# Kernel tuning notes

Measured on AMD Instinct MI355X. Metric: run time of the kernel, lower is better.

The kernel has to match this reference:

```python
import jax, jax.numpy as jnp
import numpy as np

HEAD_SIZE = 128
BLOCK_SIZE = 2048


def setup_inputs() -> dict:
    key = jax.random.key(0)
    k1, k2 = jax.random.split(key)
    B, T, D = 8, 2048, 1024
    x = jax.random.normal(k1, (B, T, D), dtype=jnp.float32)
    # Linear(dim, 3*head_size, bias=False): weight [3*head_size, dim], applied as x @ W.T
    W_qkv = jax.random.normal(k2, (3 * HEAD_SIZE, D), dtype=jnp.float32) * (1.0 / np.sqrt(D))
    return {"x": x, "W_qkv": W_qkv}


def reference(x, W_qkv):
    B, T, D = x.shape
    qkv = jnp.einsum('btd,hd->bth', x, W_qkv)  # [B, T, 3*head_size]
    q = qkv[:, :, :HEAD_SIZE]
    k = qkv[:, :, HEAD_SIZE:2 * HEAD_SIZE]
    v = qkv[:, :, 2 * HEAD_SIZE:]
    scale = 1.0 / np.sqrt(HEAD_SIZE).astype(np.float32)
    score = jnp.einsum('bqh,bkh->bqk', q, k) * scale  # [B, T, T]
    causal = jnp.tril(jnp.ones((T, T), dtype=bool))
    score = jnp.where(causal, score, -jnp.inf)
    attn = jax.nn.softmax(score, axis=-1)
    # dropout p=0.0 (eval) -> identity
    return jnp.einsum('bqk,bkh->bqh', attn, v)  # [B, T, head_size]
```

## Files before the change

kernel.cpp:

```cpp
#include <hip/hip_runtime.h>
#include <hip/hip_bf16.h>
#include <math.h>

#define D_MODEL 1024
#define TLEN    2048

typedef __attribute__((ext_vector_type(8))) short short8;
typedef __attribute__((ext_vector_type(4))) float f32x4;

static __device__ __forceinline__ unsigned short f2bf(float f) {
    __hip_bfloat16 h = __float2bfloat16(f);
    return __builtin_bit_cast(unsigned short, h);
}
static __device__ __forceinline__ float bf2f(unsigned short u) {
    unsigned int x = ((unsigned int)u) << 16;
    return __builtin_bit_cast(float, x);
}
static __device__ __forceinline__ void lds_cp16(void* lds, const void* g) {
    __builtin_amdgcn_global_load_lds(
        (const __attribute__((address_space(1))) unsigned int*)g,
        (__attribute__((address_space(3))) unsigned int*)lds, 16, 0, 0);
}

__global__ __launch_bounds__(256) void pack_w(const float* __restrict__ W,
                                              unsigned short* __restrict__ wt) {
    const int id = blockIdx.x * 256 + threadIdx.x;
    const int h  = id >> 7;
    const int kg = id & 127;
    const int k0 = kg * 8;
    const int kt = k0 >> 6;
    const int kin = k0 & 63;
    const int np = h >> 7;
    const int hp = h & 127;
    const float4 a = *(const float4*)&W[(size_t)h * D_MODEL + k0];
    const float4 b = *(const float4*)&W[(size_t)h * D_MODEL + k0 + 4];
    short8 v;
    v[0] = (short)f2bf(a.x); v[1] = (short)f2bf(a.y);
    v[2] = (short)f2bf(a.z); v[3] = (short)f2bf(a.w);
    v[4] = (short)f2bf(b.x); v[5] = (short)f2bf(b.y);
    v[6] = (short)f2bf(b.z); v[7] = (short)f2bf(b.w);
    const size_t dst = ((size_t)(np * 16 + kt) * 128 + hp) * 64 + (kin ^ ((hp & 7) * 8));
    *(short8*)&wt[dst] = v;
}

__global__ __launch_bounds__(256, 4) void qkv_gemm(const float* __restrict__ x,
                                                   const unsigned short* __restrict__ wt,
                                                   unsigned short* __restrict__ qk,
                                                   unsigned short* __restrict__ vt) {
    __shared__ unsigned short As[64][88];
    __shared__ unsigned short Bs[128 * 64];

    const int tid  = threadIdx.x;
    const int lane = tid & 63;
    const int w    = tid >> 6;
    const int wm   = w >> 1, wn = w & 1;
    const int cc   = lane & 15, g = lane >> 4;
    const int row0 = blockIdx.x * 64;
    const int np   = blockIdx.y;

    const int xr  = tid >> 2;
    const int xc0 = (tid & 3) * 16;

    const f32x4 zero = {0.f, 0.f, 0.f, 0.f};
    f32x4 acc[2][4];
#pragma unroll
    for (int i = 0; i < 2; ++i)
#pragma unroll
        for (int j = 0; j < 4; ++j) acc[i][j] = zero;

    const float* xrow = x + (size_t)(row0 + xr) * D_MODEL + xc0;
    float4 xa[4];
#pragma unroll
    for (int i = 0; i < 4; ++i) xa[i] = *(const float4*)(xrow + i * 4);

    const unsigned short* wtile0 =
        wt + (size_t)np * 16 * 128 * 64 + (w * 4 * 1024 + lane * 16) / 2;
    unsigned short* bdst = Bs + (w * 4 * 1024) / 2;

    for (int kt = 0; kt < 16; ++kt) {
        __syncthreads();
        {
            short8 s0, s1;
            s0[0] = (short)f2bf(xa[0].x); s0[1] = (short)f2bf(xa[0].y);
            s0[2] = (short)f2bf(xa[0].z); s0[3] = (short)f2bf(xa[0].w);
            s0[4] = (short)f2bf(xa[1].x); s0[5] = (short)f2bf(xa[1].y);
            s0[6] = (short)f2bf(xa[1].z); s0[7] = (short)f2bf(xa[1].w);
            s1[0] = (short)f2bf(xa[2].x); s1[1] = (short)f2bf(xa[2].y);
            s1[2] = (short)f2bf(xa[2].z); s1[3] = (short)f2bf(xa[2].w);
            s1[4] = (short)f2bf(xa[3].x); s1[5] = (short)f2bf(xa[3].y);
            s1[6] = (short)f2bf(xa[3].z); s1[7] = (short)f2bf(xa[3].w);
            *(short8*)&As[xr][xc0]     = s0;
            *(short8*)&As[xr][xc0 + 8] = s1;
        }
        const unsigned short* wtk = wtile0 + (size_t)kt * 128 * 64;
#pragma unroll
        for (int i = 0; i < 4; ++i)
            lds_cp16(bdst + i * 512, wtk + i * 512);
        __syncthreads();

        short8 af[2][2], bf[2][4];
#pragma unroll
        for (int ks = 0; ks < 2; ++ks) {
#pragma unroll
            for (int mt = 0; mt < 2; ++mt)
                af[ks][mt] = *(const short8*)&As[wm * 32 + mt * 16 + cc][ks * 32 + g * 8];
#pragma unroll
            for (int nt = 0; nt < 4; ++nt) {
                const int h = wn * 64 + nt * 16 + cc;
                bf[ks][nt] = *(const short8*)&Bs[h * 64 + (((ks * 4 + g) ^ (h & 7)) << 3)];
            }
        }
        if (kt + 1 < 16) {
#pragma unroll
            for (int i = 0; i < 4; ++i)
                xa[i] = *(const float4*)(xrow + (kt + 1) * 64 + i * 4);
        }
        __builtin_amdgcn_s_setprio(1);
#pragma unroll
        for (int ks = 0; ks < 2; ++ks)
#pragma unroll
            for (int mt = 0; mt < 2; ++mt)
#pragma unroll
                for (int nt = 0; nt < 4; ++nt)
                    acc[mt][nt] = __builtin_amdgcn_mfma_f32_16x16x32_bf16(
                        af[ks][mt], bf[ks][nt], acc[mt][nt], 0, 0, 0);
        __builtin_amdgcn_s_setprio(0);
    }

    const int bb  = row0 >> 11;
    const int tr0 = row0 & 2047;
    const float qs = (np == 0) ? 0.08838834764831845f : 1.0f;
#pragma unroll
    for (int mt = 0; mt < 2; ++mt)
#pragma unroll
        for (int nt = 0; nt < 4; ++nt) {
            const int colp = wn * 64 + nt * 16;
            if (np < 2) {
#pragma unroll
                for (int r = 0; r < 4; ++r) {
                    const int row = row0 + wm * 32 + mt * 16 + g * 4 + r;
                    qk[(size_t)row * 256 + np * 128 + colp + cc] = f2bf(acc[mt][nt][r] * qs);
                }
            } else {
                const int d    = colp + cc;
                const int trow = tr0 + wm * 32 + mt * 16 + g * 4;
                ushort4 u;
                u.x = f2bf(acc[mt][nt][0]);
                u.y = f2bf(acc[mt][nt][1]);
                u.z = f2bf(acc[mt][nt][2]);
                u.w = f2bf(acc[mt][nt][3]);
                *(ushort4*)&vt[((size_t)(bb * 128 + d)) * TLEN + trow] = u;
            }
        }
}

__global__ __launch_bounds__(256, 3) void attn_part(const unsigned short* __restrict__ qk,
                                                    const unsigned short* __restrict__ vt,
                                                    unsigned short* __restrict__ po,
                                                    float2* __restrict__ ml) {
    __shared__ unsigned short Ks[64 * 128];
    __shared__ unsigned short Vs[128 * 64];
    __shared__ unsigned short Ps[4][16][72];

    const int tid  = threadIdx.x;
    const int lane = tid & 63;
    const int w    = tid >> 6;
    const int cc   = lane & 15, g = lane >> 4;
    const int bx   = blockIdx.x;
    const int qt   = 31 - (bx / 3);
    const int ggg  = bx % 3;
    const int b    = blockIdx.y;
    const int q0   = qt * 64;
    const int slot = (b * 32 + qt) * 3 + ggg;
    const int n    = qt + 1;
    const int cnt  = (n > ggg) ? ((n - ggg + 2) / 3) : 0;

    if (cnt == 0) {
#pragma unroll
        for (int nt = 0; nt < 8; ++nt)
#pragma unroll
            for (int r = 0; r < 4; ++r)
                po[((size_t)slot * 64 + w * 16 + g * 4 + r) * 128 + nt * 16 + cc] = 0;
        if (g == 0) ml[slot * 64 + w * 16 + cc] = make_float2(-INFINITY, 0.f);
        return;
    }

    short8 qf[4];
    {
        const unsigned short* qb =
            qk + ((size_t)(b * TLEN + q0 + w * 16 + cc)) * 256 + g * 8;
#pragma unroll
        for (int kt = 0; kt < 4; ++kt) qf[kt] = *(const short8*)(qb + kt * 32);
    }

    const f32x4 zero = {0.f, 0.f, 0.f, 0.f};
    f32x4 o[8];
#pragma unroll
    for (int nt = 0; nt < 8; ++nt) o[nt] = zero;
    float mrun = -INFINITY, lrun = 0.f;

    int koff[4], voff[2];
#pragma unroll
    for (int kt = 0; kt < 4; ++kt)
        koff[kt] = cc * 128 + (((kt * 4 + g) ^ (cc & 7)) << 3);
#pragma unroll
    for (int ks = 0; ks < 2; ++ks)
        voff[ks] = cc * 64 + (((ks * 4 + g) ^ (cc & 7)) << 3);

    const int kRow = tid >> 2;
    const int kG0  = (tid & 3) * 4;
    const int vRow = tid >> 1;
    const int vG0  = (tid & 1) * 4;
    const unsigned short* kgp = qk + ((size_t)(b * TLEN + kRow)) * 256 + 128 + kG0 * 8;
    const unsigned short* vgp = vt + ((size_t)(b * 128 + vRow)) * TLEN + vG0 * 8;

    short8 kr[4], vr[4];
#pragma unroll
    for (int i = 0; i < 4; ++i) kr[i] = *(const short8*)(kgp + (size_t)ggg * 16384 + i * 8);
#pragma unroll
    for (int i = 0; i < 4; ++i) vr[i] = *(const short8*)(vgp + ggg * 64 + i * 8);

    for (int s = 0; s < cnt; ++s) {
        const int t  = 3 * s + ggg;
        const int j0 = t * 64;
        __syncthreads();
#pragma unroll
        for (int i = 0; i < 4; ++i) {
            *(short8*)&Ks[kRow * 128 + (((kG0 + i) ^ (kRow & 7)) << 3)] = kr[i];
            *(short8*)&Vs[vRow * 64  + (((vG0 + i) ^ (vRow & 7)) << 3)] = vr[i];
        }
        __syncthreads();
        if (s + 1 < cnt) {
            const int tn = t + 3;
#pragma unroll
            for (int i = 0; i < 4; ++i) kr[i] = *(const short8*)(kgp + (size_t)tn * 16384 + i * 8);
#pragma unroll
            for (int i = 0; i < 4; ++i) vr[i] = *(const short8*)(vgp + tn * 64 + i * 8);
        }

        f32x4 st[4];
#pragma unroll
        for (int jt = 0; jt < 4; ++jt) st[jt] = zero;
        __builtin_amdgcn_s_setprio(1);
#pragma unroll
        for (int kt = 0; kt < 4; ++kt)
#pragma unroll
            for (int jt = 0; jt < 4; ++jt) {
                const short8 kf = *(const short8*)&Ks[koff[kt] + jt * 2048];
                st[jt] = __builtin_amdgcn_mfma_f32_16x16x32_bf16(kf, qf[kt], st[jt], 0, 0, 0);
            }
        __builtin_amdgcn_s_setprio(0);

        if (t == qt) {
            const int qg = q0 + w * 16 + cc;
            const int jb = j0 + 4 * g;
#pragma unroll
            for (int jt = 0; jt < 4; ++jt)
#pragma unroll
                for (int r = 0; r < 4; ++r)
                    if (jb + jt * 16 + r > qg) st[jt][r] = -INFINITY;
        }
        float pmax = -INFINITY;
#pragma unroll
        for (int jt = 0; jt < 4; ++jt) {
            const float a = fmaxf(st[jt][0], st[jt][1]);
            const float c = fmaxf(st[jt][2], st[jt][3]);
            pmax = fmaxf(pmax, fmaxf(a, c));
        }
        pmax = fmaxf(pmax, __shfl_xor(pmax, 16));
        pmax = fmaxf(pmax, __shfl_xor(pmax, 32));

        if (!__all(pmax <= mrun + 8.f)) {
            const float newm  = fmaxf(mrun, pmax);
            const float alpha = __expf(mrun - newm);
            mrun = newm;
            lrun *= alpha;
            float arow[4];
#pragma unroll
            for (int r = 0; r < 4; ++r) arow[r] = __shfl(alpha, 20 * g + r);
#pragma unroll
            for (int nt = 0; nt < 8; ++nt)
#pragma unroll
                for (int r = 0; r < 4; ++r) o[nt][r] *= arow[r];
        }

        float rs = 0.f;
#pragma unroll
        for (int jt = 0; jt < 4; ++jt) {
            const float p0 = __expf(st[jt][0] - mrun);
            const float p1 = __expf(st[jt][1] - mrun);
            const float p2 = __expf(st[jt][2] - mrun);
            const float p3 = __expf(st[jt][3] - mrun);
            rs += (p0 + p1) + (p2 + p3);
            uint2 pw;
            pw.x = (unsigned int)f2bf(p0) | ((unsigned int)f2bf(p1) << 16);
            pw.y = (unsigned int)f2bf(p2) | ((unsigned int)f2bf(p3) << 16);
            *(uint2*)&Ps[w][cc][jt * 16 + 4 * g] = pw;
        }
        rs += __shfl_xor(rs, 16);
        rs += __shfl_xor(rs, 32);
        lrun += rs;

        asm volatile("s_waitcnt lgkmcnt(0)" ::: "memory");
        __builtin_amdgcn_sched_barrier(0);

        __builtin_amdgcn_s_setprio(1);
#pragma unroll
        for (int ks = 0; ks < 2; ++ks) {
            const short8 pa = *(const short8*)&Ps[w][cc][ks * 32 + g * 8];
#pragma unroll
            for (int nt = 0; nt < 8; ++nt) {
                const short8 vf = *(const short8*)&Vs[voff[ks] + nt * 1024];
                o[nt] = __builtin_amdgcn_mfma_f32_16x16x32_bf16(pa, vf, o[nt], 0, 0, 0);
            }
        }
        __builtin_amdgcn_s_setprio(0);
    }

#pragma unroll
    for (int nt = 0; nt < 8; ++nt)
#pragma unroll
        for (int r = 0; r < 4; ++r)
            po[((size_t)slot * 64 + w * 16 + g * 4 + r) * 128 + nt * 16 + cc] =
                f2bf(o[nt][r]);
    if (g == 0) ml[slot * 64 + w * 16 + cc] = make_float2(mrun, lrun);
}

__global__ __launch_bounds__(256) void attn_merge(const unsigned short* __restrict__ po,
                                                  const float2* __restrict__ ml,
                                                  float* __restrict__ out) {
    const int bq   = blockIdx.x;
    const int row  = threadIdx.x >> 2;
    const int cs   = (threadIdx.x & 3) * 32;
    const int slot = bq * 3;

    const float2 ml0 = ml[(size_t)(slot + 0) * 64 + row];
    const float2 ml1 = ml[(size_t)(slot + 1) * 64 + row];
    const float2 ml2 = ml[(size_t)(slot + 2) * 64 + row];
    const float M  = fmaxf(fmaxf(ml0.x, ml1.x), ml2.x);
    float e0 = __expf(ml0.x - M);
    float e1 = __expf(ml1.x - M);
    float e2 = __expf(ml2.x - M);
    const float inv = 1.f / (ml0.y * e0 + ml1.y * e1 + ml2.y * e2);
    e0 *= inv; e1 *= inv; e2 *= inv;

    const unsigned short* p0 = po + ((size_t)(slot + 0) * 64 + row) * 128 + cs;
    const unsigned short* p1 = po + ((size_t)(slot + 1) * 64 + row) * 128 + cs;
    const unsigned short* p2 = po + ((size_t)(slot + 2) * 64 + row) * 128 + cs;
    float* op = out + ((size_t)bq * 64 + row) * 128 + cs;

#pragma unroll
    for (int i = 0; i < 4; ++i) {
        const short8 a = *(const short8*)(p0 + i * 8);
        const short8 b = *(const short8*)(p1 + i * 8);
        const short8 c = *(const short8*)(p2 + i * 8);
        float4 o0, o1;
        o0.x = bf2f((unsigned short)a[0]) * e0 + bf2f((unsigned short)b[0]) * e1 + bf2f((unsigned short)c[0]) * e2;
        o0.y = bf2f((unsigned short)a[1]) * e0 + bf2f((unsigned short)b[1]) * e1 + bf2f((unsigned short)c[1]) * e2;
        o0.z = bf2f((unsigned short)a[2]) * e0 + bf2f((unsigned short)b[2]) * e1 + bf2f((unsigned short)c[2]) * e2;
        o0.w = bf2f((unsigned short)a[3]) * e0 + bf2f((unsigned short)b[3]) * e1 + bf2f((unsigned short)c[3]) * e2;
        o1.x = bf2f((unsigned short)a[4]) * e0 + bf2f((unsigned short)b[4]) * e1 + bf2f((unsigned short)c[4]) * e2;
        o1.y = bf2f((unsigned short)a[5]) * e0 + bf2f((unsigned short)b[5]) * e1 + bf2f((unsigned short)c[5]) * e2;
        o1.z = bf2f((unsigned short)a[6]) * e0 + bf2f((unsigned short)b[6]) * e1 + bf2f((unsigned short)c[6]) * e2;
        o1.w = bf2f((unsigned short)a[7]) * e0 + bf2f((unsigned short)b[7]) * e1 + bf2f((unsigned short)c[7]) * e2;
        *(float4*)(op + i * 8)     = o0;
        *(float4*)(op + i * 8 + 4) = o1;
    }
}

extern "C" void kernel_launch(void* const* d_in, const int* in_sizes, int n_in,
                              void* d_out, int out_size, void* d_ws, size_t ws_size,
                              hipStream_t stream) {
    (void)in_sizes; (void)n_in; (void)out_size; (void)ws_size;
    const float* x = (const float*)d_in[0];
    const float* W = (const float*)d_in[1];
    float* out = (float*)d_out;

    unsigned short* qkbf = (unsigned short*)d_ws;
    unsigned short* vtbf = qkbf + (size_t)16384 * 256;
    unsigned short* wtbf = vtbf + (size_t)8 * 128 * 2048;
    unsigned short* pobf = wtbf + (size_t)3 * 16 * 128 * 64;
    float2*         mlf  = (float2*)(pobf + (size_t)768 * 64 * 128);

    pack_w<<<dim3(192), 256, 0, stream>>>(W, wtbf);
    qkv_gemm<<<dim3(256, 3), 256, 0, stream>>>(x, wtbf, qkbf, vtbf);
    attn_part<<<dim3(96, 8), 256, 0, stream>>>(qkbf, vtbf, pobf, mlf);
    attn_merge<<<dim3(256), 256, 0, stream>>>(pobf, mlf, out);
}
```

Before: 66.78 us.

## Fuse split-KV merge into attention kernel via last-block atomic counter

Removes the separate attn_merge launch. Each of the three split blocks for a query tile bumps an atomic counter when it finishes, and the last one to arrive does the softmax-weighted merge of the partial outputs and writes the fp32 result. This saves a kernel launch and the gap between kernels, at the cost of a memset launch, an extra block barrier and fence, and some tail work on the last-arriving blocks.

```diff
diff --git a/kernel.cpp b/kernel.cpp
--- a/kernel.cpp
+++ b/kernel.cpp
@@ -157,10 +157,13 @@
 __global__ __launch_bounds__(256, 3) void attn_part(const unsigned short* __restrict__ qk,
                                                     const unsigned short* __restrict__ vt,
                                                     unsigned short* __restrict__ po,
-                                                    float2* __restrict__ ml) {
+                                                    float2* __restrict__ ml,
+                                                    float* __restrict__ out,
+                                                    int* __restrict__ cnt_g) {
     __shared__ unsigned short Ks[64 * 128];
     __shared__ unsigned short Vs[128 * 64];
     __shared__ unsigned short Ps[4][16][72];
+    __shared__ int lastflag;
 
     const int tid  = threadIdx.x;
     const int lane = tid & 63;
@@ -171,7 +174,8 @@
     const int ggg  = bx % 3;
     const int b    = blockIdx.y;
     const int q0   = qt * 64;
-    const int slot = (b * 32 + qt) * 3 + ggg;
+    const int bq   = b * 32 + qt;
+    const int slot = bq * 3 + ggg;
     const int n    = qt + 1;
     const int cnt  = (n > ggg) ? ((n - ggg + 2) / 3) : 0;
 
@@ -182,161 +186,167 @@
             for (int r = 0; r < 4; ++r)
                 po[((size_t)slot * 64 + w * 16 + g * 4 + r) * 128 + nt * 16 + cc] = 0;
         if (g == 0) ml[slot * 64 + w * 16 + cc] = make_float2(-INFINITY, 0.f);
-        return;
+    } else {
+        short8 qf[4];
+        {
+            const unsigned short* qb =
+                qk + ((size_t)(b * TLEN + q0 + w * 16 + cc)) * 256 + g * 8;
+#pragma unroll
+            for (int kt = 0; kt < 4; ++kt) qf[kt] = *(const short8*)(qb + kt * 32);
+        }
+
+        const f32x4 zero = {0.f, 0.f, 0.f, 0.f};
+        f32x4 o[8];
+#pragma unroll
+        for (int nt = 0; nt < 8; ++nt) o[nt] = zero;
+        float mrun = -INFINITY, lrun = 0.f;
+
+        int koff[4], voff[2];
+#pragma unroll
+        for (int kt = 0; kt < 4; ++kt)
+            koff[kt] = cc * 128 + (((kt * 4 + g) ^ (cc & 7)) << 3);
+#pragma unroll
+        for (int ks = 0; ks < 2; ++ks)
+            voff[ks] = cc * 64 + (((ks * 4 + g) ^ (cc & 7)) << 3);
+
+        const int kRow = tid >> 2;
+        const int kG0  = (tid & 3) * 4;
+        const int vRow = tid >> 1;
+        const int vG0  = (tid & 1) * 4;
+        const unsigned short* kgp = qk + ((size_t)(b * TLEN + kRow)) * 256 + 128 + kG0 * 8;
+        const unsigned short* vgp = vt + ((size_t)(b * 128 + vRow)) * TLEN + vG0 * 8;
+
+        short8 kr[4], vr[4];
+#pragma unroll
+        for (int i = 0; i < 4; ++i) kr[i] = *(const short8*)(kgp + (size_t)ggg * 16384 + i * 8);
+#pragma unroll
+        for (int i = 0; i < 4; ++i) vr[i] = *(const short8*)(vgp + ggg * 64 + i * 8);
+
+        for (int s = 0; s < cnt; ++s) {
+            const int t  = 3 * s + ggg;
+            const int j0 = t * 64;
+            __syncthreads();
+#pragma unroll
+            for (int i = 0; i < 4; ++i) {
+                *(short8*)&Ks[kRow * 128 + (((kG0 + i) ^ (kRow & 7)) << 3)] = kr[i];
+                *(short8*)&Vs[vRow * 64  + (((vG0 + i) ^ (vRow & 7)) << 3)] = vr[i];
+            }
+            __syncthreads();
+            if (s + 1 < cnt) {
+                const int tn = t + 3;
+#pragma unroll
+                for (int i = 0; i < 4; ++i) kr[i] = *(const short8*)(kgp + (size_t)tn * 16384 + i * 8);
+#pragma unroll
+                for (int i = 0; i < 4; ++i) vr[i] = *(const short8*)(vgp + tn * 64 + i * 8);
+            }
+
+            f32x4 st[4];
+#pragma unroll
+            for (int jt = 0; jt < 4; ++jt) st[jt] = zero;
+            __builtin_amdgcn_s_setprio(1);
+#pragma unroll
+            for (int kt = 0; kt < 4; ++kt)
+#pragma unroll
+                for (int jt = 0; jt < 4; ++jt) {
+                    const short8 kf = *(const short8*)&Ks[koff[kt] + jt * 2048];
+                    st[jt] = __builtin_amdgcn_mfma_f32_16x16x32_bf16(kf, qf[kt], st[jt], 0, 0, 0);
+                }
+            __builtin_amdgcn_s_setprio(0);
+
+            if (t == qt) {
+                const int qg = q0 + w * 16 + cc;
+                const int jb = j0 + 4 * g;
+#pragma unroll
+                for (int jt = 0; jt < 4; ++jt)
+#pragma unroll
+                    for (int r = 0; r < 4; ++r)
+                        if (jb + jt * 16 + r > qg) st[jt][r] = -INFINITY;
+            }
+            float pmax = -INFINITY;
+#pragma unroll
+            for (int jt = 0; jt < 4; ++jt) {
+                const float a = fmaxf(st[jt][0], st[jt][1]);
+                const float c = fmaxf(st[jt][2], st[jt][3]);
+                pmax = fmaxf(pmax, fmaxf(a, c));
+            }
+            pmax = fmaxf(pmax, __shfl_xor(pmax, 16));
+            pmax = fmaxf(pmax, __shfl_xor(pmax, 32));
+
+            if (!__all(pmax <= mrun + 8.f)) {
+                const float newm  = fmaxf(mrun, pmax);
+                const float alpha = __expf(mrun - newm);
+                mrun = newm;
+                lrun *= alpha;
+                float arow[4];
+#pragma unroll
+                for (int r = 0; r < 4; ++r) arow[r] = __shfl(alpha, 20 * g + r);
+#pragma unroll
+                for (int nt = 0; nt < 8; ++nt)
+#pragma unroll
+                    for (int r = 0; r < 4; ++r) o[nt][r] *= arow[r];
+            }
+
+            float rs = 0.f;
+#pragma unroll
+            for (int jt = 0; jt < 4; ++jt) {
+                const float p0 = __expf(st[jt][0] - mrun);
+                const float p1 = __expf(st[jt][1] - mrun);
+                const float p2 = __expf(st[jt][2] - mrun);
+                const float p3 = __expf(st[jt][3] - mrun);
+                rs += (p0 + p1) + (p2 + p3);
+                uint2 pw;
+                pw.x = (unsigned int)f2bf(p0) | ((unsigned int)f2bf(p1) << 16);
+                pw.y = (unsigned int)f2bf(p2) | ((unsigned int)f2bf(p3) << 16);
+                *(uint2*)&Ps[w][cc][jt * 16 + 4 * g] = pw;
+            }
+            rs += __shfl_xor(rs, 16);
+            rs += __shfl_xor(rs, 32);
+            lrun += rs;
+
+            asm volatile("s_waitcnt lgkmcnt(0)" ::: "memory");
+            __builtin_amdgcn_sched_barrier(0);
+
+            __builtin_amdgcn_s_setprio(1);
+#pragma unroll
+            for (int ks = 0; ks < 2; ++ks) {
+                const short8 pa = *(const short8*)&Ps[w][cc][ks * 32 + g * 8];
+#pragma unroll
+                for (int nt = 0; nt < 8; ++nt) {
+                    const short8 vf = *(const short8*)&Vs[voff[ks] + nt * 1024];
+                    o[nt] = __builtin_amdgcn_mfma_f32_16x16x32_bf16(pa, vf, o[nt], 0, 0, 0);
+                }
+            }
+            __builtin_amdgcn_s_setprio(0);
+        }
+
+#pragma unroll
+        for (int nt = 0; nt < 8; ++nt)
+#pragma unroll
+            for (int r = 0; r < 4; ++r)
+                po[((size_t)slot * 64 + w * 16 + g * 4 + r) * 128 + nt * 16 + cc] =
+                    f2bf(o[nt][r]);
+        if (g == 0) ml[slot * 64 + w * 16 + cc] = make_float2(mrun, lrun);
     }
 
-    short8 qf[4];
-    {
-        const unsigned short* qb =
-            qk + ((size_t)(b * TLEN + q0 + w * 16 + cc)) * 256 + g * 8;
-#pragma unroll
-        for (int kt = 0; kt < 4; ++kt) qf[kt] = *(const short8*)(qb + kt * 32);
+    __syncthreads();
+    if (tid == 0) {
+        __threadfence();
+        const int old = __hip_atomic_fetch_add(&cnt_g[bq], 1,
+                                               __ATOMIC_ACQ_REL,
+                                               __HIP_MEMORY_SCOPE_AGENT);
+        lastflag = (old == 2) ? 1 : 0;
     }
-
-    const f32x4 zero = {0.f, 0.f, 0.f, 0.f};
-    f32x4 o[8];
-#pragma unroll
-    for (int nt = 0; nt < 8; ++nt) o[nt] = zero;
-    float mrun = -INFINITY, lrun = 0.f;
-
-    int koff[4], voff[2];
-#pragma unroll
-    for (int kt = 0; kt < 4; ++kt)
-        koff[kt] = cc * 128 + (((kt * 4 + g) ^ (cc & 7)) << 3);
-#pragma unroll
-    for (int ks = 0; ks < 2; ++ks)
-        voff[ks] = cc * 64 + (((ks * 4 + g) ^ (cc & 7)) << 3);
-
-    const int kRow = tid >> 2;
-    const int kG0  = (tid & 3) * 4;
-    const int vRow = tid >> 1;
-    const int vG0  = (tid & 1) * 4;
-    const unsigned short* kgp = qk + ((size_t)(b * TLEN + kRow)) * 256 + 128 + kG0 * 8;
-    const unsigned short* vgp = vt + ((size_t)(b * 128 + vRow)) * TLEN + vG0 * 8;
-
-    short8 kr[4], vr[4];
-#pragma unroll
-    for (int i = 0; i < 4; ++i) kr[i] = *(const short8*)(kgp + (size_t)ggg * 16384 + i * 8);
-#pragma unroll
-    for (int i = 0; i < 4; ++i) vr[i] = *(const short8*)(vgp + ggg * 64 + i * 8);
-
-    for (int s = 0; s < cnt; ++s) {
-        const int t  = 3 * s + ggg;
-        const int j0 = t * 64;
-        __syncthreads();
-#pragma unroll
-        for (int i = 0; i < 4; ++i) {
-            *(short8*)&Ks[kRow * 128 + (((kG0 + i) ^ (kRow & 7)) << 3)] = kr[i];
-            *(short8*)&Vs[vRow * 64  + (((vG0 + i) ^ (vRow & 7)) << 3)] = vr[i];
-        }
-        __syncthreads();
-        if (s + 1 < cnt) {
-            const int tn = t + 3;
-#pragma unroll
-            for (int i = 0; i < 4; ++i) kr[i] = *(const short8*)(kgp + (size_t)tn * 16384 + i * 8);
-#pragma unroll
-            for (int i = 0; i < 4; ++i) vr[i] = *(const short8*)(vgp + tn * 64 + i * 8);
-        }
-
-        f32x4 st[4];
-#pragma unroll
-        for (int jt = 0; jt < 4; ++jt) st[jt] = zero;
-        __builtin_amdgcn_s_setprio(1);
-#pragma unroll
-        for (int kt = 0; kt < 4; ++kt)
-#pragma unroll
-            for (int jt = 0; jt < 4; ++jt) {
-                const short8 kf = *(const short8*)&Ks[koff[kt] + jt * 2048];
-                st[jt] = __builtin_amdgcn_mfma_f32_16x16x32_bf16(kf, qf[kt], st[jt], 0, 0, 0);
-            }
-        __builtin_amdgcn_s_setprio(0);
-
-        if (t == qt) {
-            const int qg = q0 + w * 16 + cc;
-            const int jb = j0 + 4 * g;
-#pragma unroll
-            for (int jt = 0; jt < 4; ++jt)
-#pragma unroll
-                for (int r = 0; r < 4; ++r)
-                    if (jb + jt * 16 + r > qg) st[jt][r] = -INFINITY;
-        }
-        float pmax = -INFINITY;
-#pragma unroll
-        for (int jt = 0; jt < 4; ++jt) {
-            const float a = fmaxf(st[jt][0], st[jt][1]);
-            const float c = fmaxf(st[jt][2], st[jt][3]);
-            pmax = fmaxf(pmax, fmaxf(a, c));
-        }
-        pmax = fmaxf(pmax, __shfl_xor(pmax, 16));
-        pmax = fmaxf(pmax, __shfl_xor(pmax, 32));
-
-        if (!__all(pmax <= mrun + 8.f)) {
-            const float newm  = fmaxf(mrun, pmax);
-            const float alpha = __expf(mrun - newm);
-            mrun = newm;
-            lrun *= alpha;
-            float arow[4];
-#pragma unroll
-            for (int r = 0; r < 4; ++r) arow[r] = __shfl(alpha, 20 * g + r);
-#pragma unroll
-            for (int nt = 0; nt < 8; ++nt)
-#pragma unroll
-                for (int r = 0; r < 4; ++r) o[nt][r] *= arow[r];
-        }
-
-        float rs = 0.f;
-#pragma unroll
-        for (int jt = 0; jt < 4; ++jt) {
-            const float p0 = __expf(st[jt][0] - mrun);
-            const float p1 = __expf(st[jt][1] - mrun);
-            const float p2 = __expf(st[jt][2] - mrun);
-            const float p3 = __expf(st[jt][3] - mrun);
-            rs += (p0 + p1) + (p2 + p3);
-            uint2 pw;
-            pw.x = (unsigned int)f2bf(p0) | ((unsigned int)f2bf(p1) << 16);
-            pw.y = (unsigned int)f2bf(p2) | ((unsigned int)f2bf(p3) << 16);
-            *(uint2*)&Ps[w][cc][jt * 16 + 4 * g] = pw;
-        }
-        rs += __shfl_xor(rs, 16);
-        rs += __shfl_xor(rs, 32);
-        lrun += rs;
-
-        asm volatile("s_waitcnt lgkmcnt(0)" ::: "memory");
-        __builtin_amdgcn_sched_barrier(0);
-
-        __builtin_amdgcn_s_setprio(1);
-#pragma unroll
-        for (int ks = 0; ks < 2; ++ks) {
-            const short8 pa = *(const short8*)&Ps[w][cc][ks * 32 + g * 8];
-#pragma unroll
-            for (int nt = 0; nt < 8; ++nt) {
-                const short8 vf = *(const short8*)&Vs[voff[ks] + nt * 1024];
-                o[nt] = __builtin_amdgcn_mfma_f32_16x16x32_bf16(pa, vf, o[nt], 0, 0, 0);
-            }
-        }
-        __builtin_amdgcn_s_setprio(0);
-    }
-
-#pragma unroll
-    for (int nt = 0; nt < 8; ++nt)
-#pragma unroll
-        for (int r = 0; r < 4; ++r)
-            po[((size_t)slot * 64 + w * 16 + g * 4 + r) * 128 + nt * 16 + cc] =
-                f2bf(o[nt][r]);
-    if (g == 0) ml[slot * 64 + w * 16 + cc] = make_float2(mrun, lrun);
-}
-
-__global__ __launch_bounds__(256) void attn_merge(const unsigned short* __restrict__ po,
-                                                  const float2* __restrict__ ml,
-                                                  float* __restrict__ out) {
-    const int bq   = blockIdx.x;
-    const int row  = threadIdx.x >> 2;
-    const int cs   = (threadIdx.x & 3) * 32;
-    const int slot = bq * 3;
-
-    const float2 ml0 = ml[(size_t)(slot + 0) * 64 + row];
-    const float2 ml1 = ml[(size_t)(slot + 1) * 64 + row];
-    const float2 ml2 = ml[(size_t)(slot + 2) * 64 + row];
+    __syncthreads();
+    if (lastflag == 0) return;
+    __threadfence();
+
+    const int row  = tid >> 2;
+    const int cs   = (tid & 3) * 32;
+    const int sl0  = bq * 3;
+
+    const float2 ml0 = ml[(size_t)(sl0 + 0) * 64 + row];
+    const float2 ml1 = ml[(size_t)(sl0 + 1) * 64 + row];
+    const float2 ml2 = ml[(size_t)(sl0 + 2) * 64 + row];
     const float M  = fmaxf(fmaxf(ml0.x, ml1.x), ml2.x);
     float e0 = __expf(ml0.x - M);
     float e1 = __expf(ml1.x - M);
@@ -344,25 +354,25 @@
     const float inv = 1.f / (ml0.y * e0 + ml1.y * e1 + ml2.y * e2);
     e0 *= inv; e1 *= inv; e2 *= inv;
 
-    const unsigned short* p0 = po + ((size_t)(slot + 0) * 64 + row) * 128 + cs;
-    const unsigned short* p1 = po + ((size_t)(slot + 1) * 64 + row) * 128 + cs;
-    const unsigned short* p2 = po + ((size_t)(slot + 2) * 64 + row) * 128 + cs;
+    const unsigned short* p0 = po + ((size_t)(sl0 + 0) * 64 + row) * 128 + cs;
+    const unsigned short* p1 = po + ((size_t)(sl0 + 1) * 64 + row) * 128 + cs;
+    const unsigned short* p2 = po + ((size_t)(sl0 + 2) * 64 + row) * 128 + cs;
     float* op = out + ((size_t)bq * 64 + row) * 128 + cs;
 
 #pragma unroll
     for (int i = 0; i < 4; ++i) {
         const short8 a = *(const short8*)(p0 + i * 8);
-        const short8 b = *(const short8*)(p1 + i * 8);
+        const short8 bb = *(const short8*)(p1 + i * 8);
         const short8 c = *(const short8*)(p2 + i * 8);
         float4 o0, o1;
-        o0.x = bf2f((unsigned short)a[0]) * e0 + bf2f((unsigned short)b[0]) * e1 + bf2f((unsigned short)c[0]) * e2;
-        o0.y = bf2f((unsigned short)a[1]) * e0 + bf2f((unsigned short)b[1]) * e1 + bf2f((unsigned short)c[1]) * e2;
-        o0.z = bf2f((unsigned short)a[2]) * e0 + bf2f((unsigned short)b[2]) * e1 + bf2f((unsigned short)c[2]) * e2;
-        o0.w = bf2f((unsigned short)a[3]) * e0 + bf2f((unsigned short)b[3]) * e1 + bf2f((unsigned short)c[3]) * e2;
-        o1.x = bf2f((unsigned short)a[4]) * e0 + bf2f((unsigned short)b[4]) * e1 + bf2f((unsigned short)c[4]) * e2;
-        o1.y = bf2f((unsigned short)a[5]) * e0 + bf2f((unsigned short)b[5]) * e1 + bf2f((unsigned short)c[5]) * e2;
-        o1.z = bf2f((unsigned short)a[6]) * e0 + bf2f((unsigned short)b[6]) * e1 + bf2f((unsigned short)c[6]) * e2;
-        o1.w = bf2f((unsigned short)a[7]) * e0 + bf2f((unsigned short)b[7]) * e1 + bf2f((unsigned short)c[7]) * e2;
+        o0.x = bf2f((unsigned short)a[0]) * e0 + bf2f((unsigned short)bb[0]) * e1 + bf2f((unsigned short)c[0]) * e2;
+        o0.y = bf2f((unsigned short)a[1]) * e0 + bf2f((unsigned short)bb[1]) * e1 + bf2f((unsigned short)c[1]) * e2;
+        o0.z = bf2f((unsigned short)a[2]) * e0 + bf2f((unsigned short)bb[2]) * e1 + bf2f((unsigned short)c[2]) * e2;
+        o0.w = bf2f((unsigned short)a[3]) * e0 + bf2f((unsigned short)bb[3]) * e1 + bf2f((unsigned short)c[3]) * e2;
+        o1.x = bf2f((unsigned short)a[4]) * e0 + bf2f((unsigned short)bb[4]) * e1 + bf2f((unsigned short)c[4]) * e2;
+        o1.y = bf2f((unsigned short)a[5]) * e0 + bf2f((unsigned short)bb[5]) * e1 + bf2f((unsigned short)c[5]) * e2;
+        o1.z = bf2f((unsigned short)a[6]) * e0 + bf2f((unsigned short)bb[6]) * e1 + bf2f((unsigned short)c[6]) * e2;
+        o1.w = bf2f((unsigned short)a[7]) * e0 + bf2f((unsigned short)bb[7]) * e1 + bf2f((unsigned short)c[7]) * e2;
         *(float4*)(op + i * 8)     = o0;
         *(float4*)(op + i * 8 + 4) = o1;
     }
@@ -381,9 +391,10 @@
     unsigned short* wtbf = vtbf + (size_t)8 * 128 * 2048;
     unsigned short* pobf = wtbf + (size_t)3 * 16 * 128 * 64;
     float2*         mlf  = (float2*)(pobf + (size_t)768 * 64 * 128);
-
+    int*            cntg = (int*)(mlf + (size_t)768 * 64);
+
+    hipMemsetAsync(cntg, 0, 256 * sizeof(int), stream);
     pack_w<<<dim3(192), 256, 0, stream>>>(W, wtbf);
     qkv_gemm<<<dim3(256, 3), 256, 0, stream>>>(x, wtbf, qkbf, vtbf);
-    attn_part<<<dim3(96, 8), 256, 0, stream>>>(qkbf, vtbf, pobf, mlf);
-    attn_merge<<<dim3(256), 256, 0, stream>>>(pobf, mlf, out);
-}
+    attn_part<<<dim3(96, 8), 256, 0, stream>>>(qkbf, vtbf, pobf, mlf, out, cntg);
+}
```

After: 195.2 us. 192% more time.

## Load QKV GEMM B operand directly to registers, double-buffer A in LDS

Applied to the files above, without the earlier changes.

The weight operand of the QKV projection GEMM is now kept row-major in bf16 and each lane loads its MFMA B fragments straight from global memory into registers, prefetching the next k-tile. The swizzled LDS staging tile for B is removed. The A tile is double-buffered in LDS so one barrier per iteration suffices. This saves LDS traffic and a sync, at the cost of more registers (launch bounds lowered to 3 waves) and uncoalesced 16-byte global reads of W per lane.

```diff
diff --git a/kernel.cpp b/kernel.cpp
--- a/kernel.cpp
+++ b/kernel.cpp
@@ -16,22 +16,12 @@
     unsigned int x = ((unsigned int)u) << 16;
     return __builtin_bit_cast(float, x);
 }
-static __device__ __forceinline__ void lds_cp16(void* lds, const void* g) {
-    __builtin_amdgcn_global_load_lds(
-        (const __attribute__((address_space(1))) unsigned int*)g,
-        (__attribute__((address_space(3))) unsigned int*)lds, 16, 0, 0);
-}
 
 __global__ __launch_bounds__(256) void pack_w(const float* __restrict__ W,
-                                              unsigned short* __restrict__ wt) {
+                                              unsigned short* __restrict__ wb) {
     const int id = blockIdx.x * 256 + threadIdx.x;
     const int h  = id >> 7;
-    const int kg = id & 127;
-    const int k0 = kg * 8;
-    const int kt = k0 >> 6;
-    const int kin = k0 & 63;
-    const int np = h >> 7;
-    const int hp = h & 127;
+    const int k0 = (id & 127) * 8;
     const float4 a = *(const float4*)&W[(size_t)h * D_MODEL + k0];
     const float4 b = *(const float4*)&W[(size_t)h * D_MODEL + k0 + 4];
     short8 v;
@@ -39,16 +29,14 @@
     v[2] = (short)f2bf(a.z); v[3] = (short)f2bf(a.w);
     v[4] = (short)f2bf(b.x); v[5] = (short)f2bf(b.y);
     v[6] = (short)f2bf(b.z); v[7] = (short)f2bf(b.w);
-    const size_t dst = ((size_t)(np * 16 + kt) * 128 + hp) * 64 + (kin ^ ((hp & 7) * 8));
-    *(short8*)&wt[dst] = v;
-}
-
-__global__ __launch_bounds__(256, 4) void qkv_gemm(const float* __restrict__ x,
-                                                   const unsigned short* __restrict__ wt,
+    *(short8*)&wb[(size_t)h * D_MODEL + k0] = v;
+}
+
+__global__ __launch_bounds__(256, 3) void qkv_gemm(const float* __restrict__ x,
+                                                   const unsigned short* __restrict__ wb,
                                                    unsigned short* __restrict__ qk,
                                                    unsigned short* __restrict__ vt) {
-    __shared__ unsigned short As[64][88];
-    __shared__ unsigned short Bs[128 * 64];
+    __shared__ unsigned short As[2][64][88];
 
     const int tid  = threadIdx.x;
     const int lane = tid & 63;
@@ -73,12 +61,20 @@
 #pragma unroll
     for (int i = 0; i < 4; ++i) xa[i] = *(const float4*)(xrow + i * 4);
 
-    const unsigned short* wtile0 =
-        wt + (size_t)np * 16 * 128 * 64 + (w * 4 * 1024 + lane * 16) / 2;
-    unsigned short* bdst = Bs + (w * 4 * 1024) / 2;
+    const unsigned short* bptr[4];
+#pragma unroll
+    for (int nt = 0; nt < 4; ++nt)
+        bptr[nt] = wb + (size_t)(np * 128 + wn * 64 + nt * 16 + cc) * D_MODEL + g * 8;
+
+    short8 bq[2][2][4];
+#pragma unroll
+    for (int ks = 0; ks < 2; ++ks)
+#pragma unroll
+        for (int nt = 0; nt < 4; ++nt)
+            bq[0][ks][nt] = *(const short8*)(bptr[nt] + ks * 32);
 
     for (int kt = 0; kt < 16; ++kt) {
-        __syncthreads();
+        const int cur = kt & 1;
         {
             short8 s0, s1;
             s0[0] = (short)f2bf(xa[0].x); s0[1] = (short)f2bf(xa[0].y);
@@ -89,32 +85,30 @@
             s1[2] = (short)f2bf(xa[2].z); s1[3] = (short)f2bf(xa[2].w);
             s1[4] = (short)f2bf(xa[3].x); s1[5] = (short)f2bf(xa[3].y);
             s1[6] = (short)f2bf(xa[3].z); s1[7] = (short)f2bf(xa[3].w);
-            *(short8*)&As[xr][xc0]     = s0;
-            *(short8*)&As[xr][xc0 + 8] = s1;
-        }
-        const unsigned short* wtk = wtile0 + (size_t)kt * 128 * 64;
-#pragma unroll
-        for (int i = 0; i < 4; ++i)
-            lds_cp16(bdst + i * 512, wtk + i * 512);
+            *(short8*)&As[cur][xr][xc0]     = s0;
+            *(short8*)&As[cur][xr][xc0 + 8] = s1;
+        }
         __syncthreads();
 
-        short8 af[2][2], bf[2][4];
-#pragma unroll
-        for (int ks = 0; ks < 2; ++ks) {
-#pragma unroll
-            for (int mt = 0; mt < 2; ++mt)
-                af[ks][mt] = *(const short8*)&As[wm * 32 + mt * 16 + cc][ks * 32 + g * 8];
-#pragma unroll
-            for (int nt = 0; nt < 4; ++nt) {
-                const int h = wn * 64 + nt * 16 + cc;
-                bf[ks][nt] = *(const short8*)&Bs[h * 64 + (((ks * 4 + g) ^ (h & 7)) << 3)];
-            }
-        }
         if (kt + 1 < 16) {
+#pragma unroll
+            for (int ks = 0; ks < 2; ++ks)
+#pragma unroll
+                for (int nt = 0; nt < 4; ++nt)
+                    bq[cur ^ 1][ks][nt] =
+                        *(const short8*)(bptr[nt] + (kt + 1) * 64 + ks * 32);
 #pragma unroll
             for (int i = 0; i < 4; ++i)
                 xa[i] = *(const float4*)(xrow + (kt + 1) * 64 + i * 4);
         }
+
+        short8 af[2][2];
+#pragma unroll
+        for (int ks = 0; ks < 2; ++ks)
+#pragma unroll
+            for (int mt = 0; mt < 2; ++mt)
+                af[ks][mt] = *(const short8*)&As[cur][wm * 32 + mt * 16 + cc][ks * 32 + g * 8];
+
         __builtin_amdgcn_s_setprio(1);
 #pragma unroll
         for (int ks = 0; ks < 2; ++ks)
@@ -123,7 +117,7 @@
 #pragma unroll
                 for (int nt = 0; nt < 4; ++nt)
                     acc[mt][nt] = __builtin_amdgcn_mfma_f32_16x16x32_bf16(
-                        af[ks][mt], bf[ks][nt], acc[mt][nt], 0, 0, 0);
+                        af[ks][mt], bq[cur][ks][nt], acc[mt][nt], 0, 0, 0);
         __builtin_amdgcn_s_setprio(0);
     }
 
@@ -378,12 +372,12 @@
 
     unsigned short* qkbf = (unsigned short*)d_ws;
     unsigned short* vtbf = qkbf + (size_t)16384 * 256;
-    unsigned short* wtbf = vtbf + (size_t)8 * 128 * 2048;
-    unsigned short* pobf = wtbf + (size_t)3 * 16 * 128 * 64;
+    unsigned short* wbbf = vtbf + (size_t)8 * 128 * 2048;
+    unsigned short* pobf = wbbf + (size_t)384 * 1024;
     float2*         mlf  = (float2*)(pobf + (size_t)768 * 64 * 128);
 
-    pack_w<<<dim3(192), 256, 0, stream>>>(W, wtbf);
-    qkv_gemm<<<dim3(256, 3), 256, 0, stream>>>(x, wtbf, qkbf, vtbf);
+    pack_w<<<dim3(192), 256, 0, stream>>>(W, wbbf);
+    qkv_gemm<<<dim3(256, 3), 256, 0, stream>>>(x, wbbf, qkbf, vtbf);
     attn_part<<<dim3(96, 8), 256, 0, stream>>>(qkbf, vtbf, pobf, mlf);
     attn_merge<<<dim3(256), 256, 0, stream>>>(pobf, mlf, out);
 }
```

Result: slower. 99.70 us (+49.3%).
